# Kernel optimization log

Measured on AMD Instinct MI355X. Metric: run time of the kernel, lower is better.

## Reference

```python
import jax, jax.numpy as jnp
import numpy as np

V, E, C, H = 50000, 300, 128, 128
B, SC, SE = 128, 512, 64


def gru_scan(x, lengths, gate_w, gate_b, cand_w, cand_b):
    """TF GRUCell dynamic_rnn: x [B,S,E] -> outputs [B,S,C], zeroed past lengths."""
    Bn, S, _ = x.shape
    Cn = cand_w.shape[1]

    def step(h, inp):
        xt, t = inp  # xt [B,E]
        ru = jax.nn.sigmoid(jnp.concatenate([xt, h], axis=-1) @ gate_w + gate_b)
        r, u = jnp.split(ru, 2, axis=-1)
        c = jnp.tanh(jnp.concatenate([xt, r * h], axis=-1) @ cand_w + cand_b)
        hn = u * h + (1.0 - u) * c
        active = (t < lengths)[:, None]
        hn = jnp.where(active, hn, h)
        out = jnp.where(active, hn, 0.0)
        return hn, out

    h0 = jnp.zeros((Bn, Cn), dtype=x.dtype)
    _, outs = jax.lax.scan(step, h0, (jnp.swapaxes(x, 0, 1), jnp.arange(S)))
    return jnp.swapaxes(outs, 0, 1)


def reverse_seq(x, lengths):
    """tf.reverse_sequence along time for [B,S,D]."""
    S = x.shape[1]
    t = jnp.arange(S)[None, :]
    L = lengths[:, None]
    idx = jnp.where(t < L, L - 1 - t, t)
    return jnp.take_along_axis(x, idx[:, :, None], axis=1)


def attend(states, att_v, att_w, att_b):
    # states [B,S,C]
    scores = jnp.einsum('bsd,d->bs', jnp.tanh(jnp.einsum('bsc,cd->bsd', states, att_w) + att_b), att_v)
    w = jax.nn.softmax(scores, axis=1)
    return jnp.einsum('bsc,bs->bc', states, w)


def extract_features(seq, lengths, embeddings,
                     fw_gate_w, fw_gate_b, fw_cand_w, fw_cand_b,
                     bw_gate_w, bw_gate_b, bw_cand_w, bw_cand_b,
                     att_v, att_w, att_b):
    emb = embeddings[seq]  # [B,S,E]
    fw_states = gru_scan(emb, lengths, fw_gate_w, fw_gate_b, fw_cand_w, fw_cand_b)
    emb_rev = reverse_seq(emb, lengths)
    bw_out = gru_scan(emb_rev, lengths, bw_gate_w, bw_gate_b, bw_cand_w, bw_cand_b)
    bw_states = reverse_seq(bw_out, lengths)
    fw_c = attend(fw_states, att_v, att_w, att_b)
    bw_c = attend(bw_states, att_v, att_w, att_b)
    return jnp.concatenate([fw_c, bw_c], axis=1)


def setup_inputs() -> dict:
    key = jax.random.key(0)
    ks = jax.random.split(key, 20)
    s = 0.05
    context = jax.random.randint(ks[0], (B, SC), 0, V, dtype=jnp.int32)
    end = jax.random.randint(ks[1], (B, SE), 0, V, dtype=jnp.int32)
    context_length = jnp.clip(jax.random.randint(ks[2], (B,), 1, SC + 1), 1, SC).astype(jnp.int32)
    end_length = jnp.clip(jax.random.randint(ks[3], (B,), 1, SE + 1), 1, SE).astype(jnp.int32)
    return {
        'context': context, 'end': end,
        'context_length': context_length, 'end_length': end_length,
        'embeddings': jax.random.normal(ks[4], (V, E), jnp.float32) * s,
        'fw_gate_w': jax.random.normal(ks[5], (E + C, 2 * C), jnp.float32) * s,
        'fw_gate_b': jnp.ones((2 * C,), jnp.float32),
        'fw_cand_w': jax.random.normal(ks[6], (E + C, C), jnp.float32) * s,
        'fw_cand_b': jnp.zeros((C,), jnp.float32),
        'bw_gate_w': jax.random.normal(ks[7], (E + C, 2 * C), jnp.float32) * s,
        'bw_gate_b': jnp.ones((2 * C,), jnp.float32),
        'bw_cand_w': jax.random.normal(ks[8], (E + C, C), jnp.float32) * s,
        'bw_cand_b': jnp.zeros((C,), jnp.float32),
        'att_v': jax.random.normal(ks[9], (C,), jnp.float32) * s,
        'att_w': jax.random.normal(ks[10], (C, C), jnp.float32) * s,
        'att_b': jnp.zeros((C,), jnp.float32),
        'hid_w': jax.random.normal(ks[11], (4 * C, H), jnp.float32) * s,
        'hid_b': jnp.zeros((H,), jnp.float32),
        'out_w': jax.random.normal(ks[12], (H, 1), jnp.float32) * s,
        'out_b': jnp.zeros((1,), jnp.float32),
    }


def reference(context, end, context_length, end_length, embeddings,
              fw_gate_w, fw_gate_b, fw_cand_w, fw_cand_b,
              bw_gate_w, bw_gate_b, bw_cand_w, bw_cand_b,
              att_v, att_w, att_b, hid_w, hid_b, out_w, out_b):
    ctx_f = extract_features(context, context_length, embeddings,
                             fw_gate_w, fw_gate_b, fw_cand_w, fw_cand_b,
                             bw_gate_w, bw_gate_b, bw_cand_w, bw_cand_b,
                             att_v, att_w, att_b)
    end_f = extract_features(end, end_length, embeddings,
                             fw_gate_w, fw_gate_b, fw_cand_w, fw_cand_b,
                             bw_gate_w, bw_gate_b, bw_cand_w, bw_cand_b,
                             att_v, att_w, att_b)
    feats = jnp.concatenate([ctx_f, end_f], axis=1)  # [B, 4C]
    hidden = jax.nn.relu(feats @ hid_w + hid_b)
    logit = (hidden @ out_w + out_b)[:, 0]  # [B]
    return logit
```

## Files before the change

### kernel.cpp

```cpp
#include <hip/hip_runtime.h>
#include <cstdint>
#include <cmath>

static constexpr int V_  = 50000;
static constexpr int E_  = 300;
static constexpr int C_  = 128;
static constexpr int B_  = 128;
static constexpr int SC_ = 512;
static constexpr int SE_ = 64;
static constexpr int NCOL = 768;
static constexpr int KP  = 320;

static constexpr size_t OFF_PROJ  = 0;
static constexpr size_t SZ_PROJ   = (size_t)V_ * NCOL;
static constexpr size_t OFF_WXP   = OFF_PROJ + SZ_PROJ;
static constexpr size_t SZ_WXP    = (size_t)304 * NCOL;
static constexpr size_t OFF_UALL  = OFF_WXP + SZ_WXP;
static constexpr size_t SZ_UALL   = (size_t)C_ * NCOL;
static constexpr size_t OFF_BIAS  = OFF_UALL + SZ_UALL;
static constexpr size_t SZ_BIAS   = NCOL;
static constexpr size_t OFF_ST    = OFF_BIAS + SZ_BIAS;
static constexpr size_t SZ_ST_CTX = (size_t)B_ * SC_ * C_;
static constexpr size_t SZ_ST_END = (size_t)B_ * SE_ * C_;
static constexpr size_t SZ_ST     = 2*SZ_ST_CTX + 2*SZ_ST_END;
static constexpr size_t OFF_FEATS = OFF_ST + SZ_ST;
static constexpr size_t SZ_FEATS  = (size_t)B_ * 512;
static constexpr size_t OFF_BT    = OFF_FEATS + SZ_FEATS;
static constexpr size_t SZ_BT     = (size_t)NCOL * KP / 2 * 2;
static constexpr size_t OFF_AWT   = OFF_BT + SZ_BT;

typedef __attribute__((ext_vector_type(8))) short bf16x8;
typedef __attribute__((ext_vector_type(4))) float f32x4;

static __device__ __forceinline__ unsigned short f2bf_rne(float f) {
  unsigned u = __float_as_uint(f);
  unsigned r = u + 0x7fffu + ((u >> 16) & 1u);
  return (unsigned short)(r >> 16);
}

static __device__ __forceinline__ void gload_lds16(const short* g, short* l) {
  __builtin_amdgcn_global_load_lds(
      (const __attribute__((address_space(1))) void*)g,
      (__attribute__((address_space(3))) void*)l, 16, 0, 0);
}

static __device__ __forceinline__ float fast_sigmoid(float x) {
  return __builtin_amdgcn_rcpf(1.f + __expf(-x));
}
static __device__ __forceinline__ float fast_tanh(float x) {
  return fmaf(-2.f, __builtin_amdgcn_rcpf(__expf(2.f * x) + 1.f), 1.f);
}

__global__ void pack_kernel(const float* __restrict__ fw_gw, const float* __restrict__ fw_gb,
                            const float* __restrict__ fw_cw, const float* __restrict__ fw_cb,
                            const float* __restrict__ bw_gw, const float* __restrict__ bw_gb,
                            const float* __restrict__ bw_cw, const float* __restrict__ bw_cb,
                            float* __restrict__ ws) {
  int i = blockIdx.x * 256 + threadIdx.x;
  float* Wxp  = ws + OFF_WXP;
  float* Uall = ws + OFF_UALL;
  float* bias = ws + OFF_BIAS;
  if (i < 304 * NCOL) {
    int k = i / NCOL, c = i % NCOL;
    float v = 0.f;
    if (k < 300) {
      if (c < 256)      v = fw_gw[k*256 + c];
      else if (c < 384) v = fw_cw[k*128 + (c-256)];
      else if (c < 640) v = bw_gw[k*256 + (c-384)];
      else              v = bw_cw[k*128 + (c-640)];
    }
    Wxp[i] = v;
    return;
  }
  int j = i - 304 * NCOL;
  if (j >= 0 && j < 128 * NCOL) {
    int k = j / NCOL, c = j % NCOL;
    int kk = 300 + k;
    float v;
    if (c < 256)      v = fw_gw[kk*256 + c];
    else if (c < 384) v = fw_cw[kk*128 + (c-256)];
    else if (c < 640) v = bw_gw[kk*256 + (c-384)];
    else              v = bw_cw[kk*128 + (c-640)];
    Uall[j] = v;
    return;
  }
  int m = j - 128 * NCOL;
  if (m >= 0 && m < NCOL) {
    float v;
    if (m < 256)      v = fw_gb[m];
    else if (m < 384) v = fw_cb[m-256];
    else if (m < 640) v = bw_gb[m-384];
    else              v = bw_cb[m-640];
    bias[m] = v;
  }
}

__global__ void pack_bt(const float* __restrict__ Wxp, short* __restrict__ Bthi,
                        short* __restrict__ Btlo, const float* __restrict__ att_w,
                        short* __restrict__ awt_hi, short* __restrict__ awt_lo) {
  int i = blockIdx.x * 256 + threadIdx.x;
  if (i < NCOL * KP) {
    int k = i % KP, n = i / KP;
    float v = (k < 304) ? Wxp[(size_t)k * NCOL + n] : 0.f;
    unsigned short h = f2bf_rne(v);
    float hf = __uint_as_float((unsigned)h << 16);
    unsigned short lo = f2bf_rne(v - hf);
    Bthi[i] = (short)h;
    Btlo[i] = (short)lo;
    return;
  }
  int j = i - NCOL * KP;
  if (j < 128 * 128) {
    int d = j >> 7, c = j & 127;
    float v = att_w[(size_t)c * 128 + d];
    unsigned short h = f2bf_rne(v);
    float hf = __uint_as_float((unsigned)h << 16);
    unsigned short lo = f2bf_rne(v - hf);
    awt_hi[j] = (short)h;
    awt_lo[j] = (short)lo;
  }
}

__global__ void pack_emb(const float* __restrict__ emb, short* __restrict__ Ahi,
                         short* __restrict__ Alo) {
  size_t i = (size_t)blockIdx.x * 256 + threadIdx.x;
  if (i >= (size_t)V_ * KP) return;
  int k = (int)(i % KP);
  size_t row = i / KP;
  float v = (k < E_) ? emb[row * E_ + k] : 0.f;
  unsigned short h = f2bf_rne(v);
  float hf = __uint_as_float((unsigned)h << 16);
  unsigned short lo = f2bf_rne(v - hf);
  Ahi[i] = (short)h;
  Alo[i] = (short)lo;
}

__global__ __launch_bounds__(256) void gemm_mfma(
    const short* __restrict__ Ahi, const short* __restrict__ Alo,
    const short* __restrict__ Bthi, const short* __restrict__ Btlo,
    float* __restrict__ proj) {
  __shared__ short lds[16384];
  int tid = threadIdx.x, wid = tid >> 6, lane = tid & 63;

  int bid = blockIdx.x;
  int xcd = bid & 7, idx = bid >> 3;
  int wgid = (xcd < 2 ? xcd * 294 : 588 + (xcd - 2) * 293) + idx;
  int m0 = (wgid / 6) * 128;
  int n0 = (wgid % 6) * 128;

  f32x4 acc[4][4] = {};

  int lr = lane >> 2, lc = lane & 3;
  int q0 = wid * 2, q1 = q0 + 1;
  int r0 = q0 * 16 + lr, r1 = q1 * 16 + lr;
  int am0 = m0 + r0; if (am0 > V_ - 1) am0 = V_ - 1;
  int am1 = m0 + r1; if (am1 > V_ - 1) am1 = V_ - 1;
  size_t gaOff0 = (size_t)am0 * KP + lc * 8;
  size_t gaOff1 = (size_t)am1 * KP + lc * 8;
  size_t gbOff0 = (size_t)(n0 + r0) * KP + lc * 8;
  size_t gbOff1 = (size_t)(n0 + r1) * KP + lc * 8;

  int quad = lane >> 4;
  int arow = (wid >> 1) * 64 + (lane & 15);
  int brow = (wid & 1) * 64 + (lane & 15);

  for (int k0 = 0; k0 < KP; k0 += 32) {
    gload_lds16(Ahi  + gaOff0 + k0, lds +         q0 * 512);
    gload_lds16(Ahi  + gaOff1 + k0, lds +         q1 * 512);
    gload_lds16(Alo  + gaOff0 + k0, lds +  4096 + q0 * 512);
    gload_lds16(Alo  + gaOff1 + k0, lds +  4096 + q1 * 512);
    gload_lds16(Bthi + gbOff0 + k0, lds +  8192 + q0 * 512);
    gload_lds16(Bthi + gbOff1 + k0, lds +  8192 + q1 * 512);
    gload_lds16(Btlo + gbOff0 + k0, lds + 12288 + q0 * 512);
    gload_lds16(Btlo + gbOff1 + k0, lds + 12288 + q1 * 512);
    __syncthreads();

    bf16x8 ah[4], al[4], bh[4], bl[4];
#pragma unroll
    for (int i = 0; i < 4; ++i) {
      ah[i] = *(bf16x8*)&lds[        (arow + i*16) * 32 + quad * 8];
      al[i] = *(bf16x8*)&lds[ 4096 + (arow + i*16) * 32 + quad * 8];
      bh[i] = *(bf16x8*)&lds[ 8192 + (brow + i*16) * 32 + quad * 8];
      bl[i] = *(bf16x8*)&lds[12288 + (brow + i*16) * 32 + quad * 8];
    }
#pragma unroll
    for (int i = 0; i < 4; ++i)
#pragma unroll
      for (int j = 0; j < 4; ++j) {
        acc[i][j] = __builtin_amdgcn_mfma_f32_16x16x32_bf16(ah[i], bh[j], acc[i][j], 0, 0, 0);
        acc[i][j] = __builtin_amdgcn_mfma_f32_16x16x32_bf16(ah[i], bl[j], acc[i][j], 0, 0, 0);
        acc[i][j] = __builtin_amdgcn_mfma_f32_16x16x32_bf16(al[i], bh[j], acc[i][j], 0, 0, 0);
      }
    __syncthreads();
  }

  int colb = n0 + (wid & 1) * 64 + (lane & 15);
  int rowb = m0 + (wid >> 1) * 64 + quad * 4;
#pragma unroll
  for (int i = 0; i < 4; ++i) {
    int rb = rowb + i * 16;
#pragma unroll
    for (int j = 0; j < 4; ++j) {
      int cc = colb + j * 16;
#pragma unroll
      for (int r = 0; r < 4; ++r) {
        int rr = rb + r;
        if (rr < V_) proj[(size_t)rr * NCOL + cc] = acc[i][j][r];
      }
    }
  }
}

__global__ __attribute__((amdgpu_flat_work_group_size(256, 256),
                          amdgpu_waves_per_eu(2, 2)))
void recur_kernel(
    const int* __restrict__ ctx, const int* __restrict__ endseq,
    const int* __restrict__ ctx_len, const int* __restrict__ end_len,
    const float* __restrict__ proj, const float* __restrict__ Uall,
    const float* __restrict__ bias, float* __restrict__ states) {
  __shared__ __align__(16) float h_s[128];
  __shared__ __align__(16) float rh_s[128];
  __shared__ __align__(16) float u_s[128];
  __shared__ __align__(16) float pg[8][260];
  __shared__ __align__(16) float pc[8][132];

  int bid = blockIdx.x;
  int tid = threadIdx.x;
  const int* seq; int S, L, b, dir; float* stbase;
  if (bid < 256) {
    b = bid >> 1; dir = bid & 1;
    seq = ctx + b * SC_; S = SC_; L = ctx_len[b];
    stbase = states + (dir ? SZ_ST_CTX : 0) + (size_t)b * SC_ * C_;
  } else {
    int q = bid - 256; b = q >> 1; dir = q & 1;
    seq = endseq + b * SE_; S = SE_; L = end_len[b];
    stbase = states + 2*SZ_ST_CTX + (dir ? SZ_ST_END : 0) + (size_t)b * SE_ * C_;
  }
  int dirOff = dir ? 384 : 0;
  int kg = tid >> 5, jg = tid & 31;

  float wg[16][8];
  float wc[16][4];
#pragma unroll
  for (int kk = 0; kk < 16; ++kk) {
    const float* up = Uall + (size_t)(kg*16 + kk) * NCOL + dirOff;
    float4 w0 = *(const float4*)(up + jg*8);
    float4 w1 = *(const float4*)(up + jg*8 + 4);
    wg[kk][0]=w0.x; wg[kk][1]=w0.y; wg[kk][2]=w0.z; wg[kk][3]=w0.w;
    wg[kk][4]=w1.x; wg[kk][5]=w1.y; wg[kk][6]=w1.z; wg[kk][7]=w1.w;
    float4 wv = *(const float4*)(up + 256 + jg*4);
    wc[kk][0]=wv.x; wc[kk][1]=wv.y; wc[kk][2]=wv.z; wc[kk][3]=wv.w;
  }
  float bias_g = bias[dirOff + tid];
  float bias_c = (tid < 128) ? bias[dirOff + 256 + tid] : 0.f;

  if (tid < 128) h_s[tid] = 0.f;
  __syncthreads();

  int pos0 = dir ? (L - 1) : 0;
  int tok0 = seq[pos0];
  const float* xr0 = proj + (size_t)tok0 * NCOL + dirOff;
  float xg = xr0[tid];
  float xc = (tid < 128) ? xr0[256 + tid] : 0.f;

  for (int t = 0; t < L; ++t) {
    float xg_n = 0.f, xc_n = 0.f;
    if (t + 1 < L) {
      int pos_n = dir ? (L - 2 - t) : (t + 1);
      int tok_n = seq[pos_n];
      const float* xr = proj + (size_t)tok_n * NCOL + dirOff;
      xg_n = xr[tid];
      xc_n = (tid < 128) ? xr[256 + tid] : 0.f;
    }

    float a[8] = {0.f,0.f,0.f,0.f,0.f,0.f,0.f,0.f};
    const float4* h4 = (const float4*)h_s;
#pragma unroll
    for (int q = 0; q < 4; ++q) {
      float4 hv = h4[kg*4 + q];
      float he[4] = {hv.x, hv.y, hv.z, hv.w};
#pragma unroll
      for (int e = 0; e < 4; ++e)
#pragma unroll
        for (int jj = 0; jj < 8; ++jj)
          a[jj] += he[e] * wg[q*4 + e][jj];
    }
    *(float4*)(&pg[kg][jg*8])     = make_float4(a[0], a[1], a[2], a[3]);
    *(float4*)(&pg[kg][jg*8 + 4]) = make_float4(a[4], a[5], a[6], a[7]);
    __syncthreads();

    float g = xg + bias_g;
#pragma unroll
    for (int k2 = 0; k2 < 8; ++k2) g += pg[k2][tid];
    g = fast_sigmoid(g);

    float h_old = 0.f;
    if (tid < 128) { h_old = h_s[tid]; rh_s[tid] = g * h_old; }
    else           { u_s[tid - 128] = g; }
    __syncthreads();

    float ac[4] = {0.f, 0.f, 0.f, 0.f};
    const float4* rh4 = (const float4*)rh_s;
#pragma unroll
    for (int q = 0; q < 4; ++q) {
      float4 rv = rh4[kg*4 + q];
      float re[4] = {rv.x, rv.y, rv.z, rv.w};
#pragma unroll
      for (int e = 0; e < 4; ++e)
#pragma unroll
        for (int jj = 0; jj < 4; ++jj)
          ac[jj] += re[e] * wc[q*4 + e][jj];
    }
    *(float4*)(&pc[kg][jg*4]) = make_float4(ac[0], ac[1], ac[2], ac[3]);
    __syncthreads();

    if (tid < 128) {
      float cs = xc + bias_c;
#pragma unroll
      for (int k2 = 0; k2 < 8; ++k2) cs += pc[k2][tid];
      float c = fast_tanh(cs);
      float u = u_s[tid];
      float hn = u * h_old + (1.f - u) * c;
      h_s[tid] = hn;
      int pos = dir ? (L - 1 - t) : t;
      stbase[(size_t)pos * C_ + tid] = hn;
    }
    __syncthreads();
    xg = xg_n; xc = xc_n;
  }

  for (int i = L * C_ + tid; i < S * C_; i += 256) stbase[i] = 0.f;
}

__global__ __launch_bounds__(256, 3) void attn_kernel(
    const float* __restrict__ states, const short* __restrict__ awt_hi,
    const short* __restrict__ awt_lo, const float* __restrict__ att_v,
    const float* __restrict__ att_b, float* __restrict__ partials) {
  __shared__ __align__(16) float st_s[16][132];
  __shared__ __align__(16) short ah_s[16][132];
  __shared__ __align__(16) short al_s[16][132];
  __shared__ float spart[4][16];
  __shared__ float score_s[16];
  __shared__ float cm[128], cl[128], ca[128];

  int bid = blockIdx.x, tid = threadIdx.x;
  int b, dir, S, pchain, ph, ch0, ch1, isEndWG; const float* stb;
  if (bid < 512) {
    int chain = bid >> 1;  ph = bid & 1;
    b = chain >> 1; dir = chain & 1; S = SC_;
    stb = states + (dir ? SZ_ST_CTX : 0) + (size_t)b * SC_ * C_;
    pchain = chain; ch0 = ph * 16; ch1 = ch0 + 16; isEndWG = 0;
  } else {
    int e = bid - 512;
    b = e >> 1; dir = e & 1; S = SE_;
    stb = states + 2*SZ_ST_CTX + (dir ? SZ_ST_END : 0) + (size_t)b * SE_ * C_;
    pchain = 256 + e; ph = 0; ch0 = 0; ch1 = SE_ >> 4; isEndWG = 1;
  }
  (void)S;

  int w = tid >> 6, lane = tid & 63;
  int quad = lane >> 4, l15 = lane & 15;

  int d0 = 32 * w + l15, d1 = d0 + 16;
  bf16x8 bh0[4], bh1[4], bl0[4], bl1[4];
#pragma unroll
  for (int kt = 0; kt < 4; ++kt) {
    bh0[kt] = *(const bf16x8*)&awt_hi[d0*128 + kt*32 + quad*8];
    bh1[kt] = *(const bf16x8*)&awt_hi[d1*128 + kt*32 + quad*8];
    bl0[kt] = *(const bf16x8*)&awt_lo[d0*128 + kt*32 + quad*8];
    bl1[kt] = *(const bf16x8*)&awt_lo[d1*128 + kt*32 + quad*8];
  }
  float vv0 = att_v[d0], vv1 = att_v[d1];
  float bb0 = att_b[d0], bb1 = att_b[d1];

  int c = tid & 127, half = tid >> 7;
  float m = -1e30f, lsum = 0.f, acc = 0.f;

  int lrow = tid >> 4, lcol = (tid & 15) * 8;
  float4 p0, p1;
  {
    const float* src = stb + (size_t)(ch0 * 16 + lrow) * C_ + lcol;
    p0 = *(const float4*)(src);
    p1 = *(const float4*)(src + 4);
  }

  for (int ch = ch0; ch < ch1; ++ch) {
    __syncthreads();
    float f[8] = {p0.x, p0.y, p0.z, p0.w, p1.x, p1.y, p1.z, p1.w};
    short hi8[8], lo8[8];
#pragma unroll
    for (int j = 0; j < 8; ++j) {
      unsigned short h = f2bf_rne(f[j]);
      float hf = __uint_as_float((unsigned)h << 16);
      hi8[j] = (short)h;
      lo8[j] = (short)f2bf_rne(f[j] - hf);
    }
    *(float4*)(&st_s[lrow][lcol])     = p0;
    *(float4*)(&st_s[lrow][lcol + 4]) = p1;
    *(bf16x8*)(&ah_s[lrow][lcol]) = *(bf16x8*)hi8;
    *(bf16x8*)(&al_s[lrow][lcol]) = *(bf16x8*)lo8;
    if (ch + 1 < ch1) {
      const float* src = stb + (size_t)((ch + 1) * 16 + lrow) * C_ + lcol;
      p0 = *(const float4*)(src);
      p1 = *(const float4*)(src + 4);
    }
    __syncthreads();

    f32x4 ac0 = {0.f, 0.f, 0.f, 0.f}, ac1 = {0.f, 0.f, 0.f, 0.f};
#pragma unroll
    for (int kt = 0; kt < 4; ++kt) {
      bf16x8 a_hi = *(bf16x8*)&ah_s[l15][kt*32 + quad*8];
      bf16x8 a_lo = *(bf16x8*)&al_s[l15][kt*32 + quad*8];
      ac0 = __builtin_amdgcn_mfma_f32_16x16x32_bf16(a_hi, bh0[kt], ac0, 0, 0, 0);
      ac0 = __builtin_amdgcn_mfma_f32_16x16x32_bf16(a_hi, bl0[kt], ac0, 0, 0, 0);
      ac0 = __builtin_amdgcn_mfma_f32_16x16x32_bf16(a_lo, bh0[kt], ac0, 0, 0, 0);
      ac1 = __builtin_amdgcn_mfma_f32_16x16x32_bf16(a_hi, bh1[kt], ac1, 0, 0, 0);
      ac1 = __builtin_amdgcn_mfma_f32_16x16x32_bf16(a_hi, bl1[kt], ac1, 0, 0, 0);
      ac1 = __builtin_amdgcn_mfma_f32_16x16x32_bf16(a_lo, bh1[kt], ac1, 0, 0, 0);
    }

    float part[4];
#pragma unroll
    for (int r = 0; r < 4; ++r)
      part[r] = fast_tanh(ac0[r] + bb0) * vv0 + fast_tanh(ac1[r] + bb1) * vv1;
#pragma unroll
    for (int mask = 1; mask <= 8; mask <<= 1)
#pragma unroll
      for (int r = 0; r < 4; ++r)
        part[r] += __shfl_xor(part[r], mask, 64);
    if (l15 == 0) {
#pragma unroll
      for (int r = 0; r < 4; ++r) spart[w][quad*4 + r] = part[r];
    }
    __syncthreads();
    if (tid < 16)
      score_s[tid] = spart[0][tid] + spart[1][tid] + spart[2][tid] + spart[3][tid];
    __syncthreads();

    float srow[8]; float smax = m;
#pragma unroll
    for (int r = 0; r < 8; ++r) { srow[r] = score_s[half*8 + r]; smax = fmaxf(smax, srow[r]); }
    float scale = __expf(m - smax);
    acc *= scale; lsum *= scale; m = smax;
#pragma unroll
    for (int r = 0; r < 8; ++r) {
      float wgt = __expf(srow[r] - m);
      lsum += wgt;
      acc += wgt * st_s[half*8 + r][c];
    }
  }

  __syncthreads();
  if (half == 1) { cm[c] = m; cl[c] = lsum; ca[c] = acc; }
  __syncthreads();
  if (half == 0) {
    float m1 = cm[c], l1 = cl[c], a1 = ca[c];
    float M = fmaxf(m, m1);
    float w0 = __expf(m - M), w1 = __expf(m1 - M);
    float Lt = lsum * w0 + l1 * w1;
    float At = acc * w0 + a1 * w1;
    float* p = partials + ((size_t)pchain * 2 + ph) * 130;
    if (c == 0) { p[0] = M; p[1] = Lt; }
    p[2 + c] = At;
    if (isEndWG) {
      float* pn = partials + ((size_t)pchain * 2 + 1) * 130;
      if (c == 0) { pn[0] = -1e30f; pn[1] = 0.f; }
      pn[2 + c] = 0.f;
    }
  }
}

__global__ __launch_bounds__(128) void attn_merge_kernel(
    const float* __restrict__ partials, float* __restrict__ feats) {
  int q = blockIdx.x, c = threadIdx.x;
  const float* p0 = partials + (size_t)q * 2 * 130;
  const float* p1 = p0 + 130;
  float m0 = p0[0], l0 = p0[1], a0 = p0[2 + c];
  float m1 = p1[0], l1 = p1[1], a1 = p1[2 + c];
  float M = fmaxf(m0, m1);
  float w0 = __expf(m0 - M), w1 = __expf(m1 - M);
  int b, off;
  if (q < 256) { b = q >> 1; off = (q & 1) * 128; }
  else { int e = q - 256; b = e >> 1; off = 256 + (e & 1) * 128; }
  feats[b * 512 + off + c] = (a0 * w0 + a1 * w1) / (l0 * w0 + l1 * w1);
}

__global__ __launch_bounds__(128) void head_kernel(
    const float* __restrict__ feats, const float* __restrict__ hid_w,
    const float* __restrict__ hid_b, const float* __restrict__ out_w,
    const float* __restrict__ out_b, float* __restrict__ out) {
  __shared__ __align__(16) float f_s[512];
  __shared__ float part[2];
  int b = blockIdx.x, tid = threadIdx.x;
  for (int i = tid; i < 512; i += 128) f_s[i] = feats[b * 512 + i];
  __syncthreads();
  float h = hid_b[tid];
  for (int k = 0; k < 512; ++k) h += f_s[k] * hid_w[k * 128 + tid];
  h = fmaxf(h, 0.f);
  float p = h * out_w[tid];
#pragma unroll
  for (int off = 32; off > 0; off >>= 1) p += __shfl_xor(p, off, 64);
  if ((tid & 63) == 0) part[tid >> 6] = p;
  __syncthreads();
  if (tid == 0) out[b] = part[0] + part[1] + out_b[0];
}

extern "C" void kernel_launch(void* const* d_in, const int* in_sizes, int n_in,
                              void* d_out, int out_size, void* d_ws, size_t ws_size,
                              hipStream_t stream) {
  const int*   ctx     = (const int*)d_in[0];
  const int*   endseq  = (const int*)d_in[1];
  const int*   ctx_len = (const int*)d_in[2];
  const int*   end_len = (const int*)d_in[3];
  const float* emb     = (const float*)d_in[4];
  const float* fw_gw   = (const float*)d_in[5];
  const float* fw_gb   = (const float*)d_in[6];
  const float* fw_cw   = (const float*)d_in[7];
  const float* fw_cb   = (const float*)d_in[8];
  const float* bw_gw   = (const float*)d_in[9];
  const float* bw_gb   = (const float*)d_in[10];
  const float* bw_cw   = (const float*)d_in[11];
  const float* bw_cb   = (const float*)d_in[12];
  const float* att_v   = (const float*)d_in[13];
  const float* att_w   = (const float*)d_in[14];
  const float* att_b   = (const float*)d_in[15];
  const float* hid_w   = (const float*)d_in[16];
  const float* hid_b   = (const float*)d_in[17];
  const float* out_w   = (const float*)d_in[18];
  const float* out_b   = (const float*)d_in[19];
  float* ws  = (float*)d_ws;
  float* out = (float*)d_out;

  short* Ahi    = (short*)(ws + OFF_ST);
  short* Alo    = Ahi + (size_t)V_ * KP;
  short* Bthi   = (short*)(ws + OFF_BT);
  short* Btlo   = Bthi + (size_t)NCOL * KP;
  short* awt_hi = (short*)(ws + OFF_AWT);
  short* awt_lo = awt_hi + 128 * 128;
  float* partials = ws + OFF_BT;

  pack_kernel<<<1299, 256, 0, stream>>>(fw_gw, fw_gb, fw_cw, fw_cb,
                                        bw_gw, bw_gb, bw_cw, bw_cb, ws);
  pack_bt<<<(NCOL * KP + 128 * 128 + 255) / 256, 256, 0, stream>>>(
      ws + OFF_WXP, Bthi, Btlo, att_w, awt_hi, awt_lo);
  pack_emb<<<(int)(((size_t)V_ * KP + 255) / 256), 256, 0, stream>>>(emb, Ahi, Alo);

  gemm_mfma<<<2346, 256, 0, stream>>>(Ahi, Alo, Bthi, Btlo, ws + OFF_PROJ);

  recur_kernel<<<512, 256, 0, stream>>>(ctx, endseq, ctx_len, end_len,
                                        ws + OFF_PROJ, ws + OFF_UALL,
                                        ws + OFF_BIAS, ws + OFF_ST);

  attn_kernel<<<768, 256, 0, stream>>>(ws + OFF_ST, awt_hi, awt_lo,
                                       att_v, att_b, partials);
  attn_merge_kernel<<<512, 128, 0, stream>>>(partials, ws + OFF_FEATS);

  head_kernel<<<128, 128, 0, stream>>>(ws + OFF_FEATS, hid_w, hid_b,
                                       out_w, out_b, out);
}
```

Baseline: 739.9 us.

## Hold full weight columns per thread in GRU recurrence to drop partial-sum reductions

```diff
diff --git a/kernel.cpp b/kernel.cpp
--- a/kernel.cpp
+++ b/kernel.cpp
@@ -220,9 +220,7 @@
     const float* __restrict__ bias, float* __restrict__ states) {
   __shared__ __align__(16) float h_s[128];
   __shared__ __align__(16) float rh_s[128];
-  __shared__ __align__(16) float u_s[128];
-  __shared__ __align__(16) float pg[8][260];
-  __shared__ __align__(16) float pc[8][132];
+  __shared__ float u_s[128];
 
   int bid = blockIdx.x;
   int tid = threadIdx.x;
@@ -237,22 +235,19 @@
     stbase = states + 2*SZ_ST_CTX + (dir ? SZ_ST_END : 0) + (size_t)b * SE_ * C_;
   }
   int dirOff = dir ? 384 : 0;
-  int kg = tid >> 5, jg = tid & 31;
-
-  float wg[16][8];
-  float wc[16][4];
-#pragma unroll
-  for (int kk = 0; kk < 16; ++kk) {
-    const float* up = Uall + (size_t)(kg*16 + kk) * NCOL + dirOff;
-    float4 w0 = *(const float4*)(up + jg*8);
-    float4 w1 = *(const float4*)(up + jg*8 + 4);
-    wg[kk][0]=w0.x; wg[kk][1]=w0.y; wg[kk][2]=w0.z; wg[kk][3]=w0.w;
-    wg[kk][4]=w1.x; wg[kk][5]=w1.y; wg[kk][6]=w1.z; wg[kk][7]=w1.w;
-    float4 wv = *(const float4*)(up + 256 + jg*4);
-    wc[kk][0]=wv.x; wc[kk][1]=wv.y; wc[kk][2]=wv.z; wc[kk][3]=wv.w;
-  }
+  int c = tid >> 1, p = tid & 1;
+
+  float wgt[128];
+#pragma unroll
+  for (int k = 0; k < 128; ++k)
+    wgt[k] = Uall[(size_t)k * NCOL + dirOff + tid];
+  float wct[64];
+#pragma unroll
+  for (int j = 0; j < 64; ++j)
+    wct[j] = Uall[(size_t)(p * 64 + j) * NCOL + dirOff + 256 + c];
+
   float bias_g = bias[dirOff + tid];
-  float bias_c = (tid < 128) ? bias[dirOff + 256 + tid] : 0.f;
+  float bias_c = bias[dirOff + 256 + c];
 
   if (tid < 128) h_s[tid] = 0.f;
   __syncthreads();
@@ -261,7 +256,7 @@
   int tok0 = seq[pos0];
   const float* xr0 = proj + (size_t)tok0 * NCOL + dirOff;
   float xg = xr0[tid];
-  float xc = (tid < 128) ? xr0[256 + tid] : 0.f;
+  float xc = xr0[256 + c];
 
   for (int t = 0; t < L; ++t) {
     float xg_n = 0.f, xc_n = 0.f;
@@ -270,60 +265,45 @@
       int tok_n = seq[pos_n];
       const float* xr = proj + (size_t)tok_n * NCOL + dirOff;
       xg_n = xr[tid];
-      xc_n = (tid < 128) ? xr[256 + tid] : 0.f;
-    }
-
-    float a[8] = {0.f,0.f,0.f,0.f,0.f,0.f,0.f,0.f};
+      xc_n = xr[256 + c];
+    }
+
+    float a0 = 0.f, a1 = 0.f, a2 = 0.f, a3 = 0.f;
     const float4* h4 = (const float4*)h_s;
 #pragma unroll
-    for (int q = 0; q < 4; ++q) {
-      float4 hv = h4[kg*4 + q];
-      float he[4] = {hv.x, hv.y, hv.z, hv.w};
-#pragma unroll
-      for (int e = 0; e < 4; ++e)
-#pragma unroll
-        for (int jj = 0; jj < 8; ++jj)
-          a[jj] += he[e] * wg[q*4 + e][jj];
-    }
-    *(float4*)(&pg[kg][jg*8])     = make_float4(a[0], a[1], a[2], a[3]);
-    *(float4*)(&pg[kg][jg*8 + 4]) = make_float4(a[4], a[5], a[6], a[7]);
-    __syncthreads();
-
-    float g = xg + bias_g;
-#pragma unroll
-    for (int k2 = 0; k2 < 8; ++k2) g += pg[k2][tid];
-    g = fast_sigmoid(g);
-
-    float h_old = 0.f;
-    if (tid < 128) { h_old = h_s[tid]; rh_s[tid] = g * h_old; }
-    else           { u_s[tid - 128] = g; }
-    __syncthreads();
-
-    float ac[4] = {0.f, 0.f, 0.f, 0.f};
-    const float4* rh4 = (const float4*)rh_s;
-#pragma unroll
-    for (int q = 0; q < 4; ++q) {
-      float4 rv = rh4[kg*4 + q];
-      float re[4] = {rv.x, rv.y, rv.z, rv.w};
-#pragma unroll
-      for (int e = 0; e < 4; ++e)
-#pragma unroll
-        for (int jj = 0; jj < 4; ++jj)
-          ac[jj] += re[e] * wc[q*4 + e][jj];
-    }
-    *(float4*)(&pc[kg][jg*4]) = make_float4(ac[0], ac[1], ac[2], ac[3]);
-    __syncthreads();
-
-    if (tid < 128) {
-      float cs = xc + bias_c;
-#pragma unroll
-      for (int k2 = 0; k2 < 8; ++k2) cs += pc[k2][tid];
-      float c = fast_tanh(cs);
-      float u = u_s[tid];
-      float hn = u * h_old + (1.f - u) * c;
-      h_s[tid] = hn;
+    for (int i = 0; i < 32; ++i) {
+      float4 hv = h4[i];
+      a0 = fmaf(hv.x, wgt[4*i+0], a0);
+      a1 = fmaf(hv.y, wgt[4*i+1], a1);
+      a2 = fmaf(hv.z, wgt[4*i+2], a2);
+      a3 = fmaf(hv.w, wgt[4*i+3], a3);
+    }
+    float g = fast_sigmoid((a0 + a1) + (a2 + a3) + xg + bias_g);
+
+    if (tid < 128) rh_s[tid] = g * h_s[tid];
+    else           u_s[tid - 128] = g;
+    __syncthreads();
+
+    float c0 = 0.f, c1 = 0.f, c2 = 0.f, c3 = 0.f;
+    const float4* rh4 = (const float4*)(rh_s + p * 64);
+#pragma unroll
+    for (int i = 0; i < 16; ++i) {
+      float4 rv = rh4[i];
+      c0 = fmaf(rv.x, wct[4*i+0], c0);
+      c1 = fmaf(rv.y, wct[4*i+1], c1);
+      c2 = fmaf(rv.z, wct[4*i+2], c2);
+      c3 = fmaf(rv.w, wct[4*i+3], c3);
+    }
+    float acd = (c0 + c1) + (c2 + c3);
+    acd += __shfl_xor(acd, 1, 64);
+    if (!p) {
+      float cd = fast_tanh(acd + xc + bias_c);
+      float u  = u_s[c];
+      float ho = h_s[c];
+      float hn = u * ho + (1.f - u) * cd;
+      h_s[c] = hn;
       int pos = dir ? (L - 1 - t) : t;
-      stbase[(size_t)pos * C_ + tid] = hn;
+      stbase[(size_t)pos * C_ + c] = hn;
     }
     __syncthreads();
     xg = xg_n; xc = xc_n;
```

After: 891.8 us. 20.5% more time.

## Double-buffer LDS in the embedding-projection GEMM to overlap loads with MFMA

Applied to the files above, without the earlier changes.

```diff
diff --git a/kernel.cpp b/kernel.cpp
--- a/kernel.cpp
+++ b/kernel.cpp
@@ -139,7 +139,7 @@
     const short* __restrict__ Ahi, const short* __restrict__ Alo,
     const short* __restrict__ Bthi, const short* __restrict__ Btlo,
     float* __restrict__ proj) {
-  __shared__ short lds[16384];
+  __shared__ short lds[2][16384];
   int tid = threadIdx.x, wid = tid >> 6, lane = tid & 63;
 
   int bid = blockIdx.x;
@@ -164,24 +164,32 @@
   int arow = (wid >> 1) * 64 + (lane & 15);
   int brow = (wid & 1) * 64 + (lane & 15);
 
-  for (int k0 = 0; k0 < KP; k0 += 32) {
-    gload_lds16(Ahi  + gaOff0 + k0, lds +         q0 * 512);
-    gload_lds16(Ahi  + gaOff1 + k0, lds +         q1 * 512);
-    gload_lds16(Alo  + gaOff0 + k0, lds +  4096 + q0 * 512);
-    gload_lds16(Alo  + gaOff1 + k0, lds +  4096 + q1 * 512);
-    gload_lds16(Bthi + gbOff0 + k0, lds +  8192 + q0 * 512);
-    gload_lds16(Bthi + gbOff1 + k0, lds +  8192 + q1 * 512);
-    gload_lds16(Btlo + gbOff0 + k0, lds + 12288 + q0 * 512);
-    gload_lds16(Btlo + gbOff1 + k0, lds + 12288 + q1 * 512);
-    __syncthreads();
+#define GEMM_STAGE(BUF, K0)                                          \
+  do {                                                               \
+    gload_lds16(Ahi  + gaOff0 + (K0), &lds[BUF][        q0 * 512]);  \
+    gload_lds16(Ahi  + gaOff1 + (K0), &lds[BUF][        q1 * 512]);  \
+    gload_lds16(Alo  + gaOff0 + (K0), &lds[BUF][ 4096 + q0 * 512]);  \
+    gload_lds16(Alo  + gaOff1 + (K0), &lds[BUF][ 4096 + q1 * 512]);  \
+    gload_lds16(Bthi + gbOff0 + (K0), &lds[BUF][ 8192 + q0 * 512]);  \
+    gload_lds16(Bthi + gbOff1 + (K0), &lds[BUF][ 8192 + q1 * 512]);  \
+    gload_lds16(Btlo + gbOff0 + (K0), &lds[BUF][12288 + q0 * 512]);  \
+    gload_lds16(Btlo + gbOff1 + (K0), &lds[BUF][12288 + q1 * 512]);  \
+  } while (0)
+
+  GEMM_STAGE(0, 0);
+  __syncthreads();
+
+  for (int it = 0; it < KP / 32; ++it) {
+    int cur = it & 1;
+    if (it + 1 < KP / 32) GEMM_STAGE(cur ^ 1, (it + 1) * 32);
 
     bf16x8 ah[4], al[4], bh[4], bl[4];
 #pragma unroll
     for (int i = 0; i < 4; ++i) {
-      ah[i] = *(bf16x8*)&lds[        (arow + i*16) * 32 + quad * 8];
-      al[i] = *(bf16x8*)&lds[ 4096 + (arow + i*16) * 32 + quad * 8];
-      bh[i] = *(bf16x8*)&lds[ 8192 + (brow + i*16) * 32 + quad * 8];
-      bl[i] = *(bf16x8*)&lds[12288 + (brow + i*16) * 32 + quad * 8];
+      ah[i] = *(bf16x8*)&lds[cur][        (arow + i*16) * 32 + quad * 8];
+      al[i] = *(bf16x8*)&lds[cur][ 4096 + (arow + i*16) * 32 + quad * 8];
+      bh[i] = *(bf16x8*)&lds[cur][ 8192 + (brow + i*16) * 32 + quad * 8];
+      bl[i] = *(bf16x8*)&lds[cur][12288 + (brow + i*16) * 32 + quad * 8];
     }
 #pragma unroll
     for (int i = 0; i < 4; ++i)
@@ -193,6 +201,7 @@
       }
     __syncthreads();
   }
+#undef GEMM_STAGE
 
   int colb = n0 + (wid & 1) * 64 + (lane & 15);
   int rowb = m0 + (wid >> 1) * 64 + quad * 4;
```

Measured after the change: 737.9 us. About the same (-0.3%).

## Merge weight packing kernels and stage GEMM epilogue through LDS for coalesced stores

Applied to the files above, without the earlier changes.

```diff
diff --git a/kernel.cpp b/kernel.cpp
--- a/kernel.cpp
+++ b/kernel.cpp
@@ -51,29 +51,42 @@
   return fmaf(-2.f, __builtin_amdgcn_rcpf(__expf(2.f * x) + 1.f), 1.f);
 }
 
-__global__ void pack_kernel(const float* __restrict__ fw_gw, const float* __restrict__ fw_gb,
-                            const float* __restrict__ fw_cw, const float* __restrict__ fw_cb,
-                            const float* __restrict__ bw_gw, const float* __restrict__ bw_gb,
-                            const float* __restrict__ bw_cw, const float* __restrict__ bw_cb,
-                            float* __restrict__ ws) {
+__global__ void pack_misc(const float* __restrict__ fw_gw, const float* __restrict__ fw_gb,
+                          const float* __restrict__ fw_cw, const float* __restrict__ fw_cb,
+                          const float* __restrict__ bw_gw, const float* __restrict__ bw_gb,
+                          const float* __restrict__ bw_cw, const float* __restrict__ bw_cb,
+                          const float* __restrict__ att_w,
+                          float* __restrict__ Uall, float* __restrict__ bias,
+                          short* __restrict__ Bthi, short* __restrict__ Btlo,
+                          short* __restrict__ awt_hi, short* __restrict__ awt_lo) {
   int i = blockIdx.x * 256 + threadIdx.x;
-  float* Wxp  = ws + OFF_WXP;
-  float* Uall = ws + OFF_UALL;
-  float* bias = ws + OFF_BIAS;
-  if (i < 304 * NCOL) {
-    int k = i / NCOL, c = i % NCOL;
+  if (i < NCOL * KP) {
+    int k = i % KP, n = i / KP;
     float v = 0.f;
     if (k < 300) {
-      if (c < 256)      v = fw_gw[k*256 + c];
-      else if (c < 384) v = fw_cw[k*128 + (c-256)];
-      else if (c < 640) v = bw_gw[k*256 + (c-384)];
-      else              v = bw_cw[k*128 + (c-640)];
-    }
-    Wxp[i] = v;
+      if (n < 256)      v = fw_gw[k*256 + n];
+      else if (n < 384) v = fw_cw[k*128 + (n-256)];
+      else if (n < 640) v = bw_gw[k*256 + (n-384)];
+      else              v = bw_cw[k*128 + (n-640)];
+    }
+    unsigned short h = f2bf_rne(v);
+    float hf = __uint_as_float((unsigned)h << 16);
+    Bthi[i] = (short)h;
+    Btlo[i] = (short)f2bf_rne(v - hf);
     return;
   }
-  int j = i - 304 * NCOL;
-  if (j >= 0 && j < 128 * NCOL) {
+  int j = i - NCOL * KP;
+  if (j < 128 * 128) {
+    int d = j >> 7, c = j & 127;
+    float v = att_w[(size_t)c * 128 + d];
+    unsigned short h = f2bf_rne(v);
+    float hf = __uint_as_float((unsigned)h << 16);
+    awt_hi[j] = (short)h;
+    awt_lo[j] = (short)f2bf_rne(v - hf);
+    return;
+  }
+  j -= 128 * 128;
+  if (j < 128 * NCOL) {
     int k = j / NCOL, c = j % NCOL;
     int kk = 300 + k;
     float v;
@@ -84,40 +97,14 @@
     Uall[j] = v;
     return;
   }
-  int m = j - 128 * NCOL;
-  if (m >= 0 && m < NCOL) {
+  j -= 128 * NCOL;
+  if (j < NCOL) {
     float v;
-    if (m < 256)      v = fw_gb[m];
-    else if (m < 384) v = fw_cb[m-256];
-    else if (m < 640) v = bw_gb[m-384];
-    else              v = bw_cb[m-640];
-    bias[m] = v;
-  }
-}
-
-__global__ void pack_bt(const float* __restrict__ Wxp, short* __restrict__ Bthi,
-                        short* __restrict__ Btlo, const float* __restrict__ att_w,
-                        short* __restrict__ awt_hi, short* __restrict__ awt_lo) {
-  int i = blockIdx.x * 256 + threadIdx.x;
-  if (i < NCOL * KP) {
-    int k = i % KP, n = i / KP;
-    float v = (k < 304) ? Wxp[(size_t)k * NCOL + n] : 0.f;
-    unsigned short h = f2bf_rne(v);
-    float hf = __uint_as_float((unsigned)h << 16);
-    unsigned short lo = f2bf_rne(v - hf);
-    Bthi[i] = (short)h;
-    Btlo[i] = (short)lo;
-    return;
-  }
-  int j = i - NCOL * KP;
-  if (j < 128 * 128) {
-    int d = j >> 7, c = j & 127;
-    float v = att_w[(size_t)c * 128 + d];
-    unsigned short h = f2bf_rne(v);
-    float hf = __uint_as_float((unsigned)h << 16);
-    unsigned short lo = f2bf_rne(v - hf);
-    awt_hi[j] = (short)h;
-    awt_lo[j] = (short)lo;
+    if (j < 256)      v = fw_gb[j];
+    else if (j < 384) v = fw_cb[j-256];
+    else if (j < 640) v = bw_gb[j-384];
+    else              v = bw_cb[j-640];
+    bias[j] = v;
   }
 }
 
@@ -139,7 +126,10 @@
     const short* __restrict__ Ahi, const short* __restrict__ Alo,
     const short* __restrict__ Bthi, const short* __restrict__ Btlo,
     float* __restrict__ proj) {
-  __shared__ short lds[16384];
+  __shared__ __align__(16) char smem[64 * 132 * 4];
+  short* lds = (short*)smem;
+  float (*ct)[132] = (float(*)[132])smem;
+
   int tid = threadIdx.x, wid = tid >> 6, lane = tid & 63;
 
   int bid = blockIdx.x;
@@ -194,19 +184,29 @@
     __syncthreads();
   }
 
-  int colb = n0 + (wid & 1) * 64 + (lane & 15);
-  int rowb = m0 + (wid >> 1) * 64 + quad * 4;
-#pragma unroll
-  for (int i = 0; i < 4; ++i) {
-    int rb = rowb + i * 16;
-#pragma unroll
-    for (int j = 0; j < 4; ++j) {
-      int cc = colb + j * 16;
-#pragma unroll
-      for (int r = 0; r < 4; ++r) {
-        int rr = rb + r;
-        if (rr < V_) proj[(size_t)rr * NCOL + cc] = acc[i][j][r];
-      }
+  int halfsel = wid >> 1;
+  int lcol = (wid & 1) * 64 + (lane & 15);
+#pragma unroll
+  for (int hp = 0; hp < 2; ++hp) {
+    if (hp) __syncthreads();
+    if (halfsel == hp) {
+#pragma unroll
+      for (int i = 0; i < 4; ++i)
+#pragma unroll
+        for (int j = 0; j < 4; ++j)
+#pragma unroll
+          for (int r = 0; r < 4; ++r)
+            ct[quad*4 + i*16 + r][lcol + j*16] = acc[i][j][r];
+    }
+    __syncthreads();
+#pragma unroll
+    for (int q = 0; q < 8; ++q) {
+      int f = tid + q * 256;
+      int row = f >> 5, c4 = f & 31;
+      int gr = m0 + hp * 64 + row;
+      if (gr < V_)
+        *(float4*)(proj + (size_t)gr * NCOL + n0 + c4 * 4) =
+            *(const float4*)&ct[row][c4 * 4];
     }
   }
 }
@@ -539,10 +539,10 @@
   short* awt_lo = awt_hi + 128 * 128;
   float* partials = ws + OFF_BT;
 
-  pack_kernel<<<1299, 256, 0, stream>>>(fw_gw, fw_gb, fw_cw, fw_cb,
-                                        bw_gw, bw_gb, bw_cw, bw_cb, ws);
-  pack_bt<<<(NCOL * KP + 128 * 128 + 255) / 256, 256, 0, stream>>>(
-      ws + OFF_WXP, Bthi, Btlo, att_w, awt_hi, awt_lo);
+  pack_misc<<<1411, 256, 0, stream>>>(fw_gw, fw_gb, fw_cw, fw_cb,
+                                      bw_gw, bw_gb, bw_cw, bw_cb, att_w,
+                                      ws + OFF_UALL, ws + OFF_BIAS,
+                                      Bthi, Btlo, awt_hi, awt_lo);
   pack_emb<<<(int)(((size_t)V_ * KP + 255) / 256), 256, 0, stream>>>(emb, Ahi, Alo);
 
   gemm_mfma<<<2346, 256, 0, stream>>>(Ahi, Alo, Bthi, Btlo, ws + OFF_PROJ);
```

New measurement: 756.6 us. 1.02x slower.
